# Performance work log

Measured on AMD Instinct MI355X. Metric: run time of the kernel, lower is better.

Reference implementation:

```python
import jax, jax.numpy as jnp
import numpy as np

PATCH_NUM = 10  # self.patch_num divisor
TOP_N = 5


def _extract_patches(feat, ps):
    """feat: [1,C,H,W] -> [P, C*ps*ps] with P = (H-ps)*(W-ps), matching the
    original loop over h in range(H-ps), w in range(W-ps)."""
    C, H, W = feat.shape[1:]
    Hm, Wm = H - ps, W - ps
    shifts = [feat[0, :, i:i + Hm, j:j + Wm] for i in range(ps) for j in range(ps)]
    patches = jnp.stack(shifts, axis=1)          # [C, ps*ps, Hm, Wm]
    return patches.reshape(C * ps * ps, Hm * Wm).T  # [P, K], P index = h*Wm + w


def _scale_loss(src_f, tgt_f, pos, ps):
    C = src_f.shape[1]
    K = C * ps * ps
    patches = _extract_patches(src_f, ps)  # [P, K]

    def per_target(p):
        th, tw = p[0], p[1]
        tpatch = jax.lax.dynamic_slice(tgt_f, (0, 0, th, tw), (1, C, ps, ps)).reshape(K)
        dist = jnp.sum(jnp.abs(patches - tpatch), axis=1)  # [P] summed L1 per patch
        _, ids = jax.lax.top_k(-dist, TOP_N)                # 5 nearest patches
        sel = patches[ids]                                   # [TOP_N, K]
        # sum over top-n of mean-L1, each divided by top_n (as in original)
        return jnp.sum(jnp.mean(jnp.abs(sel - tpatch), axis=1)) / TOP_N

    # sequential map over the small number of target patches keeps peak memory
    # at one [P,K] abs-diff buffer per step
    return jnp.sum(jax.lax.map(per_target, pos))


def setup_inputs() -> dict:
    key = jax.random.key(0)
    k0, k1, k2, k3, k4, k5 = jax.random.split(key, 6)
    return {
        "src_f0": jax.random.normal(k0, (1, 64, 256, 256), dtype=jnp.float32),
        "tgt_f0": jax.random.normal(k1, (1, 64, 256, 256), dtype=jnp.float32),
        "src_f1": jax.random.normal(k2, (1, 128, 128, 128), dtype=jnp.float32),
        "tgt_f1": jax.random.normal(k3, (1, 128, 128, 128), dtype=jnp.float32),
        "pos0": jax.random.randint(k4, (10, 2), 0, 253, dtype=jnp.int32),
        "pos1": jax.random.randint(k5, (5, 2), 0, 127, dtype=jnp.int32),
    }


def reference(src_f0, tgt_f0, src_f1, tgt_f1, pos0, pos1):
    loss = _scale_loss(src_f0, tgt_f0, pos0, 3) + _scale_loss(src_f1, tgt_f1, pos1, 1)
    return loss / PATCH_NUM
```

## Files before the change

kernel.cpp:

```cpp
#include <hip/hip_runtime.h>
#include <hip/hip_bf16.h>

#define BIG 3.4e38f


__device__ __forceinline__ void merge5(float a[5], const float* b) {
    float r[5];
#pragma unroll
    for (int k = 0; k < 5; ++k) {
        float best = BIG;
#pragma unroll
        for (int i = 0; i <= k + 1; ++i) {
            const int j = k + 1 - i;
            float va = (i == 0) ? -BIG : a[i - 1];
            float vb = (j == 0) ? -BIG : b[j - 1];
            best = fminf(best, fmaxf(va, vb));
        }
        r[k] = best;
    }
#pragma unroll
    for (int k = 0; k < 5; ++k) a[k] = r[k];
}

__device__ __forceinline__ void top5_insert(float m[5], float d) {
    if (d < m[4]) {
        m[4] = d;
#pragma unroll
        for (int k = 4; k > 0; --k) {
            float lo = fminf(m[k - 1], m[k]);
            float hi = fmaxf(m[k - 1], m[k]);
            m[k - 1] = lo;
            m[k] = hi;
        }
    }
}

__device__ __forceinline__ void wave_merge_top5(float m[5]) {
#pragma unroll
    for (int off = 1; off < 64; off <<= 1) {
        float o[5];
#pragma unroll
        for (int k = 0; k < 5; ++k) o[k] = __shfl_xor(m[k], off, 64);
        merge5(m, o);
    }
}

__device__ __forceinline__ bool block_merge_top5(float m[5], float (*s_top)[5],
                                                 float r[5]) {
    const int wid = threadIdx.x >> 6;
    if ((threadIdx.x & 63) == 0) {
#pragma unroll
        for (int k = 0; k < 5; ++k) s_top[wid][k] = m[k];
    }
    __syncthreads();
    if (threadIdx.x == 0) {
#pragma unroll
        for (int k = 0; k < 5; ++k) r[k] = s_top[0][k];
        merge5(r, s_top[1]);
        merge5(r, s_top[2]);
        merge5(r, s_top[3]);
        return true;
    }
    return false;
}

__global__ __launch_bounds__(256) void dist_all_kernel(
    const float* __restrict__ src0, const float* __restrict__ tgt0,
    const int* __restrict__ pos0, const float* __restrict__ src1,
    const float* __restrict__ tgt1, const int* __restrict__ pos1,
    float* __restrict__ p2a, float* __restrict__ p2b) {
    __shared__ float tl[10 * 64 * 12];
    __shared__ float sex[256 * 21];
    __shared__ float s_top[4][5];

    const int b = blockIdx.x;
    if (b < 506) {
        constexpr int W = 256, HW = 65536, T = 10;
        const int h = b >> 1;
        const int wbase = (b & 1) << 7;

        for (int idx = threadIdx.x; idx < T * 64 * 9; idx += 256) {
            int t = idx / 576;
            int rem = idx - t * 576;
            int c = rem / 9;
            int r2 = rem - c * 9;
            int i = r2 / 3, j = r2 - i * 3;
            tl[((t * 64 + c) * 3 + i) * 4 + j] =
                tgt0[(size_t)c * HW + (pos0[2 * t] + i) * W +
                     (pos0[2 * t + 1] + j)];
        }
        __syncthreads();

        const int p = threadIdx.x & 63;
        const int q = threadIdx.x >> 6;
        const int w0 = wbase + 2 * p;
        const int w0l = (w0 <= 252) ? w0 : 252;

        float acc[T][2];
#pragma unroll
        for (int t = 0; t < T; ++t) acc[t][0] = acc[t][1] = 0.f;

        const float* sb = src0 + (size_t)(q * 16) * HW + h * W + w0l;
        for (int c = 0; c < 16; ++c) {
            const float* row = sb + (size_t)c * HW;
#pragma unroll
            for (int i = 0; i < 3; ++i) {
                const float4 a = *(const float4*)(row + i * W);
#pragma unroll
                for (int t = 0; t < T; ++t) {
                    const float4 tv = *(const float4*)&tl
                        [((t * 64 + q * 16 + c) * 3 + i) * 4];
                    acc[t][0] += fabsf(a.x - tv.x) + fabsf(a.y - tv.y) +
                                 fabsf(a.z - tv.z);
                    acc[t][1] += fabsf(a.y - tv.x) + fabsf(a.z - tv.y) +
                                 fabsf(a.w - tv.z);
                }
            }
        }

        {
            float* se = &sex[threadIdx.x * 21];
#pragma unroll
            for (int t = 0; t < T; ++t) {
                se[2 * t] = acc[t][0];
                se[2 * t + 1] = acc[t][1];
            }
        }
        __syncthreads();

        for (int t = q; t < T; t += 4) {
            const int ke = 2 * t + (p & 1);
            const int pr = (p >> 1) * 21;
            float dlo = 0.f, dhi = 0.f;
#pragma unroll
            for (int qq = 0; qq < 4; ++qq) {
                dlo += sex[qq * 64 * 21 + pr + ke];
                dhi += sex[qq * 64 * 21 + 32 * 21 + pr + ke];
            }
            if (wbase + p >= 253) dlo = BIG;
            if (wbase + p + 64 >= 253) dhi = BIG;
            float m[5] = {dlo, BIG, BIG, BIG, BIG};
            top5_insert(m, dhi);
            wave_merge_top5(m);
            if (p == 0) {
                float* dst = p2a + (t * 506 + b) * 5;
#pragma unroll
                for (int k = 0; k < 5; ++k) dst[k] = m[k];
            }
        }
    } else {
        constexpr int W = 128, HW = 16384, T = 5, C = 128;
        const int bb = b - 506;
        for (int idx = threadIdx.x; idx < T * C; idx += 256) {
            int t = idx / C, cc = idx - t * C;
            tl[idx] =
                tgt1[(size_t)cc * HW + pos1[2 * t] * W + pos1[2 * t + 1]];
        }
        __syncthreads();

        const int w = threadIdx.x & 127;
        const int h = bb * 2 + (threadIdx.x >> 7);
        float acc[T] = {0.f, 0.f, 0.f, 0.f, 0.f};
        const float* sp = src1 + h * W + w;
        for (int cc = 0; cc < C; ++cc) {
            const float v = sp[(size_t)cc * HW];
#pragma unroll
            for (int t = 0; t < T; ++t) acc[t] += fabsf(v - tl[t * C + cc]);
        }
        const bool valid = (h < 127) && (w < 127);
#pragma unroll
        for (int t = 0; t < T; ++t) {
            float m[5] = {valid ? acc[t] : BIG, BIG, BIG, BIG, BIG};
            wave_merge_top5(m);
            float r[5];
            if (block_merge_top5(m, s_top, r)) {
                float* dst = p2b + (t * 64 + bb) * 5;
#pragma unroll
                for (int k = 0; k < 5; ++k) dst[k] = r[k];
            }
            __syncthreads();
        }
    }
}

__global__ __launch_bounds__(256) void final_merge_kernel(
    const float* __restrict__ p2a, int na,
    const float* __restrict__ p2b, int nb,
    unsigned int* __restrict__ out) {
    __shared__ float s_sum[15];
    const int lane = threadIdx.x & 63;
    const int wv = threadIdx.x >> 6;
#pragma unroll
    for (int rt = 0; rt < 4; ++rt) {
        const int t = wv * 4 + rt;
        if (t < 15) {
            const float* base = (t < 10) ? p2a + t * na : p2b + (t - 10) * nb;
            const int n = (t < 10) ? na : nb;
            const float scale =
                (t < 10) ? 1.f / (576.f * 5.f) : 1.f / (128.f * 5.f);
            float m[5] = {BIG, BIG, BIG, BIG, BIG};
            for (int b0 = 0; b0 < n; b0 += 256) {
                float v[4];
#pragma unroll
                for (int j = 0; j < 4; ++j) {
                    const int idx = b0 + j * 64 + lane;
                    v[j] = (idx < n) ? base[idx] : BIG;
                }
#pragma unroll
                for (int j = 0; j < 4; ++j) top5_insert(m, v[j]);
            }
            wave_merge_top5(m);
            if (lane == 0)
                s_sum[t] = (m[0] + m[1] + m[2] + m[3] + m[4]) * scale;
        }
    }
    __syncthreads();
    if (threadIdx.x == 0) {
        float total = 0.f;
#pragma unroll
        for (int t = 0; t < 15; ++t) total += s_sum[t];
        union { float f; unsigned int i; } uf;
        uf.f = total * 0.1f;
        unsigned int bf = (uf.i + 0x7FFFu + ((uf.i >> 16) & 1u)) >> 16;
        out[0] = (uf.i & 0xFFFF0000u) | (bf & 0xFFFFu);
    }
}

template <int C, int H, int PS, int WM>
__global__ __launch_bounds__(256) void dist_top5_kernel(
    const float* __restrict__ src, const float* __restrict__ tgt,
    const int* __restrict__ pos, float* __restrict__ part) {
    constexpr int W = H;
    constexpr int K = C * PS * PS;
    constexpr int P = WM * WM;
    __shared__ float tlv[K];
    __shared__ float s_top[4][5];
    const int t = blockIdx.y;
    const int th = pos[2 * t], tw = pos[2 * t + 1];
    for (int idx = threadIdx.x; idx < K; idx += 256) {
        int c = idx / (PS * PS);
        int rem = idx - c * PS * PS;
        int i = rem / PS, j = rem - i * PS;
        tlv[idx] = tgt[(c * H + th + i) * W + tw + j];
    }
    __syncthreads();
    const int p = blockIdx.x * 256 + threadIdx.x;
    float d = BIG;
    if (p < P) {
        const int h = p / WM, w = p - h * WM;
        float acc = 0.f;
        for (int c = 0; c < C; ++c)
#pragma unroll
            for (int i = 0; i < PS; ++i) {
                const float* r = src + (c * H + h + i) * W + w;
                const float* tr = &tlv[(c * PS + i) * PS];
#pragma unroll
                for (int j = 0; j < PS; ++j) acc += fabsf(r[j] - tr[j]);
            }
        d = acc;
    }
    float m[5] = {d, BIG, BIG, BIG, BIG};
    wave_merge_top5(m);
    float r[5];
    if (block_merge_top5(m, s_top, r)) {
        float* dst = part + (t * gridDim.x + blockIdx.x) * 5;
#pragma unroll
        for (int k = 0; k < 5; ++k) dst[k] = r[k];
    }
}

extern "C" void kernel_launch(void* const* d_in, const int* in_sizes, int n_in,
                              void* d_out, int out_size, void* d_ws, size_t ws_size,
                              hipStream_t stream) {
    const float* src0 = (const float*)d_in[0];
    const float* tgt0 = (const float*)d_in[1];
    const float* src1 = (const float*)d_in[2];
    const float* tgt1 = (const float*)d_in[3];
    const int* pos0 = (const int*)d_in[4];
    const int* pos1 = (const int*)d_in[5];
    unsigned int* out = (unsigned int*)d_out;

    constexpr size_t NP2A = 10 * 506 * 5;
    constexpr size_t NP2B = 5 * 64 * 5;
    const size_t need = (NP2A + NP2B) * 4;

    if (ws_size >= need) {
        float* p2a = (float*)d_ws;
        float* p2b = p2a + NP2A;

        dist_all_kernel<<<dim3(570), 256, 0, stream>>>(
            src0, tgt0, pos0, src1, tgt1, pos1, p2a, p2b);
        final_merge_kernel<<<dim3(1), 256, 0, stream>>>(
            p2a, 506 * 5, p2b, 320, out);
    } else {
        float* part0 = (float*)d_ws;
        float* part1 = part0 + 10 * 251 * 5;
        dist_top5_kernel<64, 256, 3, 253>
            <<<dim3(251, 10), 256, 0, stream>>>(src0, tgt0, pos0, part0);
        dist_top5_kernel<128, 128, 1, 127>
            <<<dim3(64, 5), 256, 0, stream>>>(src1, tgt1, pos1, part1);
        final_merge_kernel<<<dim3(1), 256, 0, stream>>>(part0, 1255, part1, 320, out);
    }
}
```

Before: 154.3 us.

## Split scale-0 distance work across more blocks with in-wave channel reduction and ballot top-5

Scale-0 work is split into four 64-column blocks per row instead of two 128-column blocks, doubling the grid. Each thread now handles one patch position and a quarter of the channels. Partial sums are combined with shuffles instead of a shared-memory exchange. Top-5 selection now uses five rounds of wave min-reduction plus a ballot, replacing the pairwise merge network, and one thread per target merges the per-wave results. The target tile gets a padded layout to avoid bank conflicts, and launch bounds request 5 blocks per CU for occupancy. In exchange, each thread loads a float4 per row but uses only three of its values, so reuse drops, and the final merge must read twice as many partials.

```diff
diff --git a/kernel.cpp b/kernel.cpp
--- a/kernel.cpp
+++ b/kernel.cpp
@@ -35,6 +35,21 @@
     }
 }
 
+__device__ __forceinline__ void wave_top5_extract(float d, int lane,
+                                                  float r[5]) {
+#pragma unroll
+    for (int k = 0; k < 5; ++k) {
+        float v = d;
+#pragma unroll
+        for (int off = 32; off >= 1; off >>= 1)
+            v = fminf(v, __shfl_xor(v, off, 64));
+        r[k] = v;
+        const unsigned long long ball = __ballot(d == v);
+        const int src = (int)__ffsll(ball) - 1;
+        if (lane == src) d = BIG;
+    }
+}
+
 __device__ __forceinline__ void wave_merge_top5(float m[5]) {
 #pragma unroll
     for (int off = 1; off < 64; off <<= 1) {
@@ -64,121 +79,131 @@
     return false;
 }
 
-__global__ __launch_bounds__(256) void dist_all_kernel(
+__global__ __launch_bounds__(256, 5) void dist_all_kernel(
     const float* __restrict__ src0, const float* __restrict__ tgt0,
     const int* __restrict__ pos0, const float* __restrict__ src1,
     const float* __restrict__ tgt1, const int* __restrict__ pos1,
     float* __restrict__ p2a, float* __restrict__ p2b) {
-    __shared__ float tl[10 * 64 * 12];
-    __shared__ float sex[256 * 21];
-    __shared__ float s_top[4][5];
+    __shared__ float tl[7696];
+    __shared__ float s_top[4][10][5];
 
     const int b = blockIdx.x;
-    if (b < 506) {
-        constexpr int W = 256, HW = 65536, T = 10;
-        const int h = b >> 1;
-        const int wbase = (b & 1) << 7;
-
-        for (int idx = threadIdx.x; idx < T * 64 * 9; idx += 256) {
-            int t = idx / 576;
-            int rem = idx - t * 576;
-            int c = rem / 9;
-            int r2 = rem - c * 9;
-            int i = r2 / 3, j = r2 - i * 3;
-            tl[((t * 64 + c) * 3 + i) * 4 + j] =
-                tgt0[(size_t)c * HW + (pos0[2 * t] + i) * W +
-                     (pos0[2 * t + 1] + j)];
+    if (b < 1012) {
+        const int h = b >> 2;
+
+        for (int t = 0; t < 10; ++t) {
+            const int th = pos0[2 * t], tw = pos0[2 * t + 1];
+            for (int inner = threadIdx.x; inner < 576; inner += 256) {
+                const int ch = inner / 9;
+                const int rr = inner - ch * 9;
+                const int i = rr / 3, j = rr - i * 3;
+                tl[t * 768 + ch * 12 + i * 4 + j + ((ch >> 4) << 2)] =
+                    tgt0[(size_t)ch * 65536 + (th + i) * 256 + (tw + j)];
+            }
         }
         __syncthreads();
 
-        const int p = threadIdx.x & 63;
-        const int q = threadIdx.x >> 6;
-        const int w0 = wbase + 2 * p;
-        const int w0l = (w0 <= 252) ? w0 : 252;
-
-        float acc[T][2];
-#pragma unroll
-        for (int t = 0; t < T; ++t) acc[t][0] = acc[t][1] = 0.f;
-
-        const float* sb = src0 + (size_t)(q * 16) * HW + h * W + w0l;
+        const int lane = threadIdx.x & 63;
+        const int wv = threadIdx.x >> 6;
+        const int pp = lane & 15;
+        const int cq = lane >> 4;
+        const int wg = ((b & 3) << 6) + wv * 16 + pp;
+        const int wp = (wg <= 252) ? wg : 252;
+
+        float acc[10];
+#pragma unroll
+        for (int t = 0; t < 10; ++t) acc[t] = 0.f;
+
+        const float* sb = src0 + (size_t)(cq * 16) * 65536 + h * 256 + wp;
+        const float* tb = tl + cq * 196;
         for (int c = 0; c < 16; ++c) {
-            const float* row = sb + (size_t)c * HW;
+            const float* row = sb + (size_t)c * 65536;
+            const float* tc = tb + c * 12;
 #pragma unroll
             for (int i = 0; i < 3; ++i) {
-                const float4 a = *(const float4*)(row + i * W);
-#pragma unroll
-                for (int t = 0; t < T; ++t) {
-                    const float4 tv = *(const float4*)&tl
-                        [((t * 64 + q * 16 + c) * 3 + i) * 4];
-                    acc[t][0] += fabsf(a.x - tv.x) + fabsf(a.y - tv.y) +
-                                 fabsf(a.z - tv.z);
-                    acc[t][1] += fabsf(a.y - tv.x) + fabsf(a.z - tv.y) +
-                                 fabsf(a.w - tv.z);
+                const float4 a = *(const float4*)(row + i * 256);
+#pragma unroll
+                for (int t = 0; t < 10; ++t) {
+                    const float4 tv = *(const float4*)(tc + t * 768 + i * 4);
+                    acc[t] += fabsf(a.x - tv.x) + fabsf(a.y - tv.y) +
+                              fabsf(a.z - tv.z);
                 }
             }
         }
 
-        {
-            float* se = &sex[threadIdx.x * 21];
-#pragma unroll
-            for (int t = 0; t < T; ++t) {
-                se[2 * t] = acc[t][0];
-                se[2 * t + 1] = acc[t][1];
+#pragma unroll
+        for (int t = 0; t < 10; ++t) {
+            float d = acc[t];
+            d += __shfl_xor(d, 16, 64);
+            d += __shfl_xor(d, 32, 64);
+            acc[t] = d;
+        }
+        const bool valid = (cq == 0) && (wg < 253);
+
+#pragma unroll
+        for (int t = 0; t < 10; ++t) {
+            float r[5];
+            wave_top5_extract(valid ? acc[t] : BIG, lane, r);
+            if (lane == 0) {
+#pragma unroll
+                for (int k = 0; k < 5; ++k) s_top[wv][t][k] = r[k];
             }
         }
         __syncthreads();
-
-        for (int t = q; t < T; t += 4) {
-            const int ke = 2 * t + (p & 1);
-            const int pr = (p >> 1) * 21;
-            float dlo = 0.f, dhi = 0.f;
-#pragma unroll
-            for (int qq = 0; qq < 4; ++qq) {
-                dlo += sex[qq * 64 * 21 + pr + ke];
-                dhi += sex[qq * 64 * 21 + 32 * 21 + pr + ke];
-            }
-            if (wbase + p >= 253) dlo = BIG;
-            if (wbase + p + 64 >= 253) dhi = BIG;
-            float m[5] = {dlo, BIG, BIG, BIG, BIG};
-            top5_insert(m, dhi);
-            wave_merge_top5(m);
-            if (p == 0) {
-                float* dst = p2a + (t * 506 + b) * 5;
-#pragma unroll
-                for (int k = 0; k < 5; ++k) dst[k] = m[k];
-            }
+        if (threadIdx.x < 10) {
+            const int t = threadIdx.x;
+            float r[5];
+#pragma unroll
+            for (int k = 0; k < 5; ++k) r[k] = s_top[0][t][k];
+            merge5(r, s_top[1][t]);
+            merge5(r, s_top[2][t]);
+            merge5(r, s_top[3][t]);
+            float* dst = p2a + (t * 1012 + b) * 5;
+#pragma unroll
+            for (int k = 0; k < 5; ++k) dst[k] = r[k];
         }
     } else {
-        constexpr int W = 128, HW = 16384, T = 5, C = 128;
-        const int bb = b - 506;
-        for (int idx = threadIdx.x; idx < T * C; idx += 256) {
-            int t = idx / C, cc = idx - t * C;
+        const int bb = b - 1012;
+        for (int idx = threadIdx.x; idx < 640; idx += 256) {
+            const int t = idx >> 7, cc = idx & 127;
             tl[idx] =
-                tgt1[(size_t)cc * HW + pos1[2 * t] * W + pos1[2 * t + 1]];
+                tgt1[(size_t)cc * 16384 + pos1[2 * t] * 128 + pos1[2 * t + 1]];
         }
         __syncthreads();
 
         const int w = threadIdx.x & 127;
-        const int h = bb * 2 + (threadIdx.x >> 7);
-        float acc[T] = {0.f, 0.f, 0.f, 0.f, 0.f};
-        const float* sp = src1 + h * W + w;
-        for (int cc = 0; cc < C; ++cc) {
-            const float v = sp[(size_t)cc * HW];
-#pragma unroll
-            for (int t = 0; t < T; ++t) acc[t] += fabsf(v - tl[t * C + cc]);
-        }
-        const bool valid = (h < 127) && (w < 127);
-#pragma unroll
-        for (int t = 0; t < T; ++t) {
-            float m[5] = {valid ? acc[t] : BIG, BIG, BIG, BIG, BIG};
-            wave_merge_top5(m);
+        const int h1 = bb * 2 + (threadIdx.x >> 7);
+        float acc[5] = {0.f, 0.f, 0.f, 0.f, 0.f};
+        const float* sp = src1 + h1 * 128 + w;
+        for (int cc = 0; cc < 128; ++cc) {
+            const float v = sp[(size_t)cc * 16384];
+#pragma unroll
+            for (int t = 0; t < 5; ++t) acc[t] += fabsf(v - tl[t * 128 + cc]);
+        }
+        const int lane = threadIdx.x & 63;
+        const int wv = threadIdx.x >> 6;
+        const bool valid = (h1 < 127) && (w < 127);
+#pragma unroll
+        for (int t = 0; t < 5; ++t) {
             float r[5];
-            if (block_merge_top5(m, s_top, r)) {
-                float* dst = p2b + (t * 64 + bb) * 5;
-#pragma unroll
-                for (int k = 0; k < 5; ++k) dst[k] = r[k];
-            }
-            __syncthreads();
+            wave_top5_extract(valid ? acc[t] : BIG, lane, r);
+            if (lane == 0) {
+#pragma unroll
+                for (int k = 0; k < 5; ++k) s_top[wv][t][k] = r[k];
+            }
+        }
+        __syncthreads();
+        if (threadIdx.x < 5) {
+            const int t = threadIdx.x;
+            float r[5];
+#pragma unroll
+            for (int k = 0; k < 5; ++k) r[k] = s_top[0][t][k];
+            merge5(r, s_top[1][t]);
+            merge5(r, s_top[2][t]);
+            merge5(r, s_top[3][t]);
+            float* dst = p2b + (t * 64 + bb) * 5;
+#pragma unroll
+            for (int k = 0; k < 5; ++k) dst[k] = r[k];
         }
     }
 }
@@ -280,7 +305,7 @@
     const int* pos1 = (const int*)d_in[5];
     unsigned int* out = (unsigned int*)d_out;
 
-    constexpr size_t NP2A = 10 * 506 * 5;
+    constexpr size_t NP2A = 10 * 1012 * 5;
     constexpr size_t NP2B = 5 * 64 * 5;
     const size_t need = (NP2A + NP2B) * 4;
 
@@ -288,10 +313,10 @@
         float* p2a = (float*)d_ws;
         float* p2b = p2a + NP2A;
 
-        dist_all_kernel<<<dim3(570), 256, 0, stream>>>(
+        dist_all_kernel<<<dim3(1076), 256, 0, stream>>>(
             src0, tgt0, pos0, src1, tgt1, pos1, p2a, p2b);
         final_merge_kernel<<<dim3(1), 256, 0, stream>>>(
-            p2a, 506 * 5, p2b, 320, out);
+            p2a, 1012 * 5, p2b, 320, out);
     } else {
         float* part0 = (float*)d_ws;
         float* part1 = part0 + 10 * 251 * 5;
```

New measurement: 255.0 us. 1.65x slower.
